# Kernel tuning notes

Hardware: AMD Instinct MI355X
Metric: run time of the kernel (lower is better)

## Reference

```python
import jax, jax.numpy as jnp
import numpy as np

N_NODES = 50000
N_EDGES = 800000
IN_DIM = 128
OUT_DIM = 128
NEG_INIT = -1e9  # matches torch fill_(-1e9) init for scatter amax
LEAKY_SLOPE = 0.01  # nn.LeakyReLU default


def setup_inputs() -> dict:
    key = jax.random.key(0)
    ks = jax.random.split(key, 8)
    x = jax.random.normal(ks[0], (N_NODES, IN_DIM), dtype=jnp.float32)
    edge_index = jax.random.randint(ks[1], (2, N_EDGES), 0, N_NODES, dtype=jnp.int64)
    edge_weight = jax.random.uniform(ks[2], (N_EDGES,), dtype=jnp.float32)
    # MLP params (nn.Linear default init: U(-1/sqrt(fan_in), 1/sqrt(fan_in)))
    s1 = 1.0 / np.sqrt(IN_DIM)
    s2 = 1.0 / np.sqrt(OUT_DIM)
    w1 = jax.random.uniform(ks[3], (OUT_DIM, IN_DIM), minval=-s1, maxval=s1, dtype=jnp.float32)
    b1 = jax.random.uniform(ks[4], (OUT_DIM,), minval=-s1, maxval=s1, dtype=jnp.float32)
    w2 = jax.random.uniform(ks[5], (OUT_DIM, OUT_DIM), minval=-s2, maxval=s2, dtype=jnp.float32)
    b2 = jax.random.uniform(ks[6], (OUT_DIM,), minval=-s2, maxval=s2, dtype=jnp.float32)
    eps = jnp.zeros((1,), dtype=jnp.float32)
    return {"x": x, "edge_index": edge_index, "edge_weight": edge_weight,
            "w1": w1, "b1": b1, "w2": w2, "b2": b2, "eps": eps}


def reference(x, edge_index, edge_weight, w1, b1, w2, b2, eps):
    src = edge_index[0]
    dst = edge_index[1]
    # gather + optional edge-weight scale: [E, D]
    messages = x[src] * edge_weight[:, None]
    # scatter-max to dst; init at -1e9 so include_self=False semantics hold
    agg = jnp.full(x.shape, NEG_INIT, dtype=x.dtype).at[dst].max(messages)
    agg = jnp.where(agg == NEG_INIT, jnp.zeros_like(agg), agg)  # isolated nodes -> 0
    h = (1.0 + eps) * x + agg  # eps broadcasts ([1])
    h = h @ w1.T + b1
    h = jnp.where(h >= 0, h, LEAKY_SLOPE * h)  # LeakyReLU
    out = h @ w2.T + b2
    return out
```

## Files before the change

kernel.cpp:

```cpp
#include <hip/hip_runtime.h>
#include <stdint.h>

#define NN 50000
#define NE 800000
#define D  128
#define NEG_INIT -1e9f
#define CAP 64
#define OVF_CAP 131072

#define CNT_OFF     64
#define OVF_CNT_OFF 50064
#define OVF_OFF     50068
#define BKT_OFF     312320
#define XBF_OFF     3512320
#define WBF_OFF     6712320

#define NBLK 196
#define HSTRIDE 136

typedef __attribute__((ext_vector_type(8))) short short8;
typedef __attribute__((ext_vector_type(4))) float float4v;

__device__ __forceinline__ float b2f(uint16_t u) {
    union { uint32_t u; float f; } v; v.u = ((uint32_t)u) << 16; return v.f;
}
__device__ __forceinline__ uint16_t f2b(float f) {
    union { float f; uint32_t u; } v; v.f = f;
    uint32_t r = v.u + 0x7fffu + ((v.u >> 16) & 1u);
    return (uint16_t)(r >> 16);
}

__device__ __forceinline__ void block_probe(const uint16_t* __restrict__ xraw,
                                            const int* __restrict__ eraw,
                                            int* sflags) {
    int t = threadIdx.x;
    if (t < 64) {
        float v0 = b2f(xraw[2 * t]);
        float v1 = b2f(xraw[2 * t + 1]);
        int bad = (!(v0 > -1e4f && v0 < 1e4f)) || (!(v1 > -1e4f && v1 < 1e4f));
        unsigned long long bm = __ballot(bad);
        int nz = (t < 32) ? (eraw[2 * t + 1] != 0) : 0;
        unsigned long long im = __ballot(nz);
        if (t == 0) { sflags[0] = bm ? 1 : 0; sflags[1] = im ? 0 : 1; }
    }
    __syncthreads();
}

__global__ __launch_bounds__(256) void prep_kernel(
    const uint16_t* __restrict__ xraw,
    const int*      __restrict__ eraw,
    const uint16_t* __restrict__ w1raw,
    const uint16_t* __restrict__ w2raw,
    int* __restrict__ ws)
{
    __shared__ int sflags[2];
    block_probe(xraw, eraw, sflags);
    const int f32 = sflags[0];

    int bid = blockIdx.x;
    if (bid < 6250) {
        int i4 = (bid * 256 + threadIdx.x) * 4;
        ushort* dst = (ushort*)(ws + XBF_OFF);
        if (f32) {
            float4 v = *(const float4*)((const float*)xraw + i4);
            ushort4 o; o.x = f2b(v.x); o.y = f2b(v.y); o.z = f2b(v.z); o.w = f2b(v.w);
            *(ushort4*)(dst + i4) = o;
        } else {
            *(ushort4*)(dst + i4) = *(const ushort4*)(xraw + i4);
        }
    } else if (bid < 6282) {
        int i4 = ((bid - 6250) * 256 + threadIdx.x) * 4;
        const uint16_t* src = (i4 < 16384) ? w1raw : w2raw;
        int off = i4 & 16383;
        ushort* dst = (ushort*)(ws + WBF_OFF);
        if (f32) {
            float4 v = *(const float4*)((const float*)src + off);
            ushort4 o; o.x = f2b(v.x); o.y = f2b(v.y); o.z = f2b(v.z); o.w = f2b(v.w);
            *(ushort4*)(dst + i4) = o;
        } else {
            *(ushort4*)(dst + i4) = *(const ushort4*)(src + off);
        }
    } else {
        int i = (bid - 6282) * 256 + threadIdx.x;
        if (i < NN) ws[CNT_OFF + i] = 0;
        if (i == 0)  ws[OVF_CNT_OFF] = 0;
    }
}

__global__ __launch_bounds__(256) void fill_kernel(
    const uint16_t* __restrict__ xraw,
    const int*      __restrict__ eraw,
    const uint16_t* __restrict__ ewraw,
    int* __restrict__ ws)
{
    __shared__ int sflags[2];
    block_probe(xraw, eraw, sflags);
    const int f32 = sflags[0], i64 = sflags[1];

    int e = blockIdx.x * 256 + threadIdx.x;
    int src, dst;
    if (i64) {
        const long long* e64 = (const long long*)eraw;
        src = (int)e64[e];
        dst = (int)e64[NE + e];
    } else {
        src = eraw[e];
        dst = eraw[NE + e];
    }
    if ((unsigned)src >= NN || (unsigned)dst >= NN) return;
    uint w = f32 ? (uint)f2b(((const float*)ewraw)[e]) : (uint)ewraw[e];
    uint entry = (w << 16) | (uint)src;
    int slot = atomicAdd(ws + CNT_OFF + dst, 1);
    if (slot < CAP) {
        ((uint*)(ws + BKT_OFF))[(size_t)dst * CAP + slot] = entry;
    } else {
        int o = atomicAdd(ws + OVF_CNT_OFF, 1);
        if (o < OVF_CAP) {
            ws[OVF_OFF + 2 * o]     = dst;
            ws[OVF_OFF + 2 * o + 1] = (int)entry;
        }
    }
}

__global__ __launch_bounds__(256) void gmlp_kernel(
    const uint16_t* __restrict__ xraw,
    const int*      __restrict__ eraw,
    const uint16_t* __restrict__ b1raw,
    const uint16_t* __restrict__ b2raw,
    const uint16_t* __restrict__ epsraw,
    const int* __restrict__ ws,
    uint16_t* __restrict__ outraw)
{
    __shared__ int    sflags[2];
    __shared__ uint   tl[16 * (HSTRIDE / 2)];
    __shared__ ushort hl[16 * HSTRIDE];

    block_probe(xraw, eraw, sflags);
    const int f32 = sflags[0];

    const int tid  = threadIdx.x;
    const int wave = tid >> 6;
    const int lane = tid & 63;
    const int m    = lane & 15;
    const int quad = lane >> 4;
    const int node0 = blockIdx.x * 16;

    const ushort* w1b = (const ushort*)(ws + WBF_OFF);
    const ushort* w2b = w1b + 16384;
    const uint*   xbf = (const uint*)(ws + XBF_OFF);
    const uint*   bkt = (const uint*)(ws + BKT_OFF);

    const float eps1 = 1.0f + (f32 ? ((const float*)epsraw)[0] : b2f(epsraw[0]));

    for (int j = 0; j < 4; ++j) {
        int nl = wave * 4 + j;
        int n  = node0 + nl;
        int cnt_raw = ws[CNT_OFF + n];
        int cnt = (cnt_raw < CAP) ? cnt_raw : CAP;

        float m0[16], m1[16];
        #pragma unroll
        for (int u = 0; u < 16; ++u) { m0[u] = NEG_INIT; m1[u] = NEG_INIT; }

        const uint* brow = bkt + (size_t)n * CAP;
        for (int i = 0; i < cnt; i += 16) {
            uint4 q[4];
            #pragma unroll
            for (int qq = 0; qq < 4; ++qq) q[qq] = *(const uint4*)(brow + i + qq * 4);
            #pragma unroll
            for (int u = 0; u < 16; ++u) {
                uint e0 = ((const uint*)q)[u];
                bool ok = (i + u) < cnt;
                uint idx = ok ? (e0 & 0xffffu) : 0u;
                uint v = xbf[idx * 64 + lane];
                float w  = b2f((uint16_t)(e0 >> 16));
                float p0 = b2f((uint16_t)v) * w;
                float p1 = b2f((uint16_t)(v >> 16)) * w;
                m0[u] = fmaxf(m0[u], ok ? p0 : NEG_INIT);
                m1[u] = fmaxf(m1[u], ok ? p1 : NEG_INIT);
            }
        }
        if (cnt_raw > CAP) {
            int novf = ws[OVF_CNT_OFF];
            if (novf > OVF_CAP) novf = OVF_CAP;
            for (int o = 0; o < novf; ++o) {
                if (ws[OVF_OFF + 2 * o] == n) {
                    uint e0 = (uint)ws[OVF_OFF + 2 * o + 1];
                    uint v  = xbf[(e0 & 0xffff) * 64 + lane];
                    float w = b2f((uint16_t)(e0 >> 16));
                    m0[0] = fmaxf(m0[0], b2f((uint16_t)v) * w);
                    m1[0] = fmaxf(m1[0], b2f((uint16_t)(v >> 16)) * w);
                }
            }
        }
        #pragma unroll
        for (int u = 8; u > 0; u >>= 1)
            #pragma unroll
            for (int v2 = 0; v2 < u; ++v2) {
                m0[v2] = fmaxf(m0[v2], m0[v2 + u]);
                m1[v2] = fmaxf(m1[v2], m1[v2 + u]);
            }
        float mx = m0[0], my = m1[0];
        if (cnt_raw == 0) { mx = 0.f; my = 0.f; }

        uint xv = xbf[(size_t)n * 64 + lane];
        float t0 = eps1 * b2f((uint16_t)xv) + mx;
        float t1 = eps1 * b2f((uint16_t)(xv >> 16)) + my;
        tl[nl * (HSTRIDE / 2) + lane] = (uint)f2b(t0) | ((uint)f2b(t1) << 16);
    }
    __syncthreads();

    short8 a[4];
    {
        const ushort* arow = (const ushort*)tl + m * HSTRIDE + quad * 8;
        #pragma unroll
        for (int kb = 0; kb < 4; ++kb) a[kb] = *(const short8*)(arow + kb * 32);
    }

    #pragma unroll
    for (int t = 0; t < 2; ++t) {
        int ct = wave * 2 + t;
        float4v c = {0.f, 0.f, 0.f, 0.f};
        const ushort* brow = w1b + (size_t)(ct * 16 + m) * 128 + quad * 8;
        #pragma unroll
        for (int kb = 0; kb < 4; ++kb)
            c = __builtin_amdgcn_mfma_f32_16x16x32_bf16(a[kb], *(const short8*)(brow + kb * 32), c, 0, 0, 0);
        float bias = f32 ? ((const float*)b1raw)[ct * 16 + m] : b2f(b1raw[ct * 16 + m]);
        #pragma unroll
        for (int r = 0; r < 4; ++r) {
            float v = c[r] + bias;
            v = (v >= 0.f) ? v : 0.01f * v;
            hl[(quad * 4 + r) * HSTRIDE + ct * 16 + m] = f2b(v);
        }
    }
    __syncthreads();

    short8 ah[4];
    {
        const ushort* hrow = hl + m * HSTRIDE + quad * 8;
        #pragma unroll
        for (int kb = 0; kb < 4; ++kb) ah[kb] = *(const short8*)(hrow + kb * 32);
    }

    #pragma unroll
    for (int t = 0; t < 2; ++t) {
        int ct = wave * 2 + t;
        float4v c = {0.f, 0.f, 0.f, 0.f};
        const ushort* brow = w2b + (size_t)(ct * 16 + m) * 128 + quad * 8;
        #pragma unroll
        for (int kb = 0; kb < 4; ++kb)
            c = __builtin_amdgcn_mfma_f32_16x16x32_bf16(ah[kb], *(const short8*)(brow + kb * 32), c, 0, 0, 0);
        float bias = f32 ? ((const float*)b2raw)[ct * 16 + m] : b2f(b2raw[ct * 16 + m]);
        #pragma unroll
        for (int r = 0; r < 4; ++r) {
            float v = c[r] + bias;
            size_t o = (size_t)(node0 + quad * 4 + r) * 128 + ct * 16 + m;
            if (f32) ((float*)outraw)[o] = v;
            else     outraw[o] = f2b(v);
        }
    }
}

extern "C" void kernel_launch(void* const* d_in, const int* in_sizes, int n_in,
                              void* d_out, int out_size, void* d_ws, size_t ws_size,
                              hipStream_t stream) {
    const uint16_t* x    = (const uint16_t*)d_in[0];
    const int*      eidx = (const int*)     d_in[1];
    const uint16_t* ew   = (const uint16_t*)d_in[2];
    const uint16_t* w1   = (const uint16_t*)d_in[3];
    const uint16_t* b1   = (const uint16_t*)d_in[4];
    const uint16_t* w2   = (const uint16_t*)d_in[5];
    const uint16_t* b2   = (const uint16_t*)d_in[6];
    const uint16_t* eps  = (const uint16_t*)d_in[7];
    uint16_t*       out  = (uint16_t*)d_out;
    int* ws = (int*)d_ws;

    prep_kernel<<<6250 + 32 + NBLK, 256, 0, stream>>>(x, eidx, w1, w2, ws);
    fill_kernel<<<NE / 256, 256, 0, stream>>>(x, eidx, ew, ws);
    gmlp_kernel<<<NN / 16, 256, 0, stream>>>(x, eidx, b1, b2, eps, ws, out);
}
```

Measured before the change: 209.8 us.

## Bucket edges by source slice so gathers sweep x in cache-friendly phases

The per-destination buckets are split into four cells, one per quarter of the source-node range, and the gather kernel walks the slices in lockstep with a block barrier after each. Blocks running together then read source rows from the same quarter of x, which is meant to keep the gather working set in L2/MALL. The inner loop is also reshaped into a 4-wide overlapping window instead of a 16-wide masked unroll. In exchange it adds four times the counters and bucket cells, more atomic contention spread, extra barriers, and a higher overflow risk, since each cell holds only 20 entries.

```diff
diff --git a/kernel.cpp b/kernel.cpp
--- a/kernel.cpp
+++ b/kernel.cpp
@@ -5,17 +5,19 @@
 #define NE 800000
 #define D  128
 #define NEG_INIT -1e9f
-#define CAP 64
+#define NS 4
+#define SLICE 12500
+#define CAPS 20
 #define OVF_CAP 131072
 
 #define CNT_OFF     64
-#define OVF_CNT_OFF 50064
-#define OVF_OFF     50068
-#define BKT_OFF     312320
-#define XBF_OFF     3512320
-#define WBF_OFF     6712320
-
-#define NBLK 196
+#define OVF_CNT_OFF 200064
+#define OVF_OFF     200068
+#define BKT_OFF     462336
+#define XBF_OFF     4462336
+#define WBF_OFF     7662336
+
+#define NBLKC 782
 #define HSTRIDE 136
 
 typedef __attribute__((ext_vector_type(8))) short short8;
@@ -82,8 +84,8 @@
         }
     } else {
         int i = (bid - 6282) * 256 + threadIdx.x;
-        if (i < NN) ws[CNT_OFF + i] = 0;
-        if (i == 0)  ws[OVF_CNT_OFF] = 0;
+        if (i < NN * NS) ws[CNT_OFF + i] = 0;
+        if (i == NN * NS) ws[OVF_CNT_OFF] = 0;
     }
 }
 
@@ -110,9 +112,11 @@
     if ((unsigned)src >= NN || (unsigned)dst >= NN) return;
     uint w = f32 ? (uint)f2b(((const float*)ewraw)[e]) : (uint)ewraw[e];
     uint entry = (w << 16) | (uint)src;
-    int slot = atomicAdd(ws + CNT_OFF + dst, 1);
-    if (slot < CAP) {
-        ((uint*)(ws + BKT_OFF))[(size_t)dst * CAP + slot] = entry;
+    int s = src / SLICE;
+    int cell = dst * NS + s;
+    int slot = atomicAdd(ws + CNT_OFF + cell, 1);
+    if (slot < CAPS) {
+        ((uint*)(ws + BKT_OFF))[(size_t)cell * CAPS + slot] = entry;
     } else {
         int o = atomicAdd(ws + OVF_CNT_OFF, 1);
         if (o < OVF_CAP) {
@@ -152,57 +156,86 @@
 
     const float eps1 = 1.0f + (f32 ? ((const float*)epsraw)[0] : b2f(epsraw[0]));
 
+    float acc0[4], acc1[4];
+    int   tot[4];
+    int   ovf_any = 0;
+    #pragma unroll
+    for (int j = 0; j < 4; ++j) { acc0[j] = NEG_INIT; acc1[j] = NEG_INIT; tot[j] = 0; }
+
+    for (int s = 0; s < NS; ++s) {
+        #pragma unroll
+        for (int j = 0; j < 4; ++j) {
+            int n = node0 + wave * 4 + j;
+            int cell = n * NS + s;
+            int cr = ws[CNT_OFF + cell];
+            tot[j] += cr;
+            if (cr > CAPS) ovf_any = 1;
+            int cc = (cr < CAPS) ? cr : CAPS;
+            const uint* brow = bkt + (size_t)cell * CAPS;
+
+            if (cc >= 4) {
+                int i = 0;
+                while (true) {
+                    uint e0 = brow[i], e1 = brow[i + 1], e2 = brow[i + 2], e3 = brow[i + 3];
+                    uint v0 = xbf[(e0 & 0xffffu) * 64 + lane];
+                    uint v1 = xbf[(e1 & 0xffffu) * 64 + lane];
+                    uint v2 = xbf[(e2 & 0xffffu) * 64 + lane];
+                    uint v3 = xbf[(e3 & 0xffffu) * 64 + lane];
+                    float w0 = b2f((uint16_t)(e0 >> 16)), w1v = b2f((uint16_t)(e1 >> 16));
+                    float w2v = b2f((uint16_t)(e2 >> 16)), w3 = b2f((uint16_t)(e3 >> 16));
+                    float q0 = fmaxf(b2f((uint16_t)v0) * w0, b2f((uint16_t)v1) * w1v);
+                    float q1 = fmaxf(b2f((uint16_t)v2) * w2v, b2f((uint16_t)v3) * w3);
+                    acc0[j] = fmaxf(acc0[j], fmaxf(q0, q1));
+                    float r0 = fmaxf(b2f((uint16_t)(v0 >> 16)) * w0, b2f((uint16_t)(v1 >> 16)) * w1v);
+                    float r1 = fmaxf(b2f((uint16_t)(v2 >> 16)) * w2v, b2f((uint16_t)(v3 >> 16)) * w3);
+                    acc1[j] = fmaxf(acc1[j], fmaxf(r0, r1));
+                    i += 4;
+                    if (i >= cc) break;
+                    if (i + 4 > cc) i = cc - 4;
+                }
+            } else if (cc > 0) {
+                uint e0 = brow[0], e1 = brow[1], e2 = brow[2], e3 = brow[3];
+                uint ee[4] = {e0, e1, e2, e3};
+                #pragma unroll
+                for (int u = 0; u < 4; ++u) {
+                    uint v = xbf[(ee[u] & 0xffffu) * 64 + lane];
+                    float w  = b2f((uint16_t)(ee[u] >> 16));
+                    bool ok = u < cc;
+                    float p0 = b2f((uint16_t)v) * w;
+                    float p1 = b2f((uint16_t)(v >> 16)) * w;
+                    acc0[j] = fmaxf(acc0[j], ok ? p0 : NEG_INIT);
+                    acc1[j] = fmaxf(acc1[j], ok ? p1 : NEG_INIT);
+                }
+            }
+        }
+        __syncthreads();
+    }
+
+    if (ovf_any) {
+        int novf = ws[OVF_CNT_OFF];
+        if (novf > OVF_CAP) novf = OVF_CAP;
+        for (int o = 0; o < novf; ++o) {
+            int dsto = ws[OVF_OFF + 2 * o];
+            #pragma unroll
+            for (int j = 0; j < 4; ++j) {
+                int n = node0 + wave * 4 + j;
+                if (dsto == n) {
+                    uint e0 = (uint)ws[OVF_OFF + 2 * o + 1];
+                    uint v  = xbf[(e0 & 0xffff) * 64 + lane];
+                    float w = b2f((uint16_t)(e0 >> 16));
+                    acc0[j] = fmaxf(acc0[j], b2f((uint16_t)v) * w);
+                    acc1[j] = fmaxf(acc1[j], b2f((uint16_t)(v >> 16)) * w);
+                }
+            }
+        }
+    }
+
+    #pragma unroll
     for (int j = 0; j < 4; ++j) {
         int nl = wave * 4 + j;
         int n  = node0 + nl;
-        int cnt_raw = ws[CNT_OFF + n];
-        int cnt = (cnt_raw < CAP) ? cnt_raw : CAP;
-
-        float m0[16], m1[16];
-        #pragma unroll
-        for (int u = 0; u < 16; ++u) { m0[u] = NEG_INIT; m1[u] = NEG_INIT; }
-
-        const uint* brow = bkt + (size_t)n * CAP;
-        for (int i = 0; i < cnt; i += 16) {
-            uint4 q[4];
-            #pragma unroll
-            for (int qq = 0; qq < 4; ++qq) q[qq] = *(const uint4*)(brow + i + qq * 4);
-            #pragma unroll
-            for (int u = 0; u < 16; ++u) {
-                uint e0 = ((const uint*)q)[u];
-                bool ok = (i + u) < cnt;
-                uint idx = ok ? (e0 & 0xffffu) : 0u;
-                uint v = xbf[idx * 64 + lane];
-                float w  = b2f((uint16_t)(e0 >> 16));
-                float p0 = b2f((uint16_t)v) * w;
-                float p1 = b2f((uint16_t)(v >> 16)) * w;
-                m0[u] = fmaxf(m0[u], ok ? p0 : NEG_INIT);
-                m1[u] = fmaxf(m1[u], ok ? p1 : NEG_INIT);
-            }
-        }
-        if (cnt_raw > CAP) {
-            int novf = ws[OVF_CNT_OFF];
-            if (novf > OVF_CAP) novf = OVF_CAP;
-            for (int o = 0; o < novf; ++o) {
-                if (ws[OVF_OFF + 2 * o] == n) {
-                    uint e0 = (uint)ws[OVF_OFF + 2 * o + 1];
-                    uint v  = xbf[(e0 & 0xffff) * 64 + lane];
-                    float w = b2f((uint16_t)(e0 >> 16));
-                    m0[0] = fmaxf(m0[0], b2f((uint16_t)v) * w);
-                    m1[0] = fmaxf(m1[0], b2f((uint16_t)(v >> 16)) * w);
-                }
-            }
-        }
-        #pragma unroll
-        for (int u = 8; u > 0; u >>= 1)
-            #pragma unroll
-            for (int v2 = 0; v2 < u; ++v2) {
-                m0[v2] = fmaxf(m0[v2], m0[v2 + u]);
-                m1[v2] = fmaxf(m1[v2], m1[v2 + u]);
-            }
-        float mx = m0[0], my = m1[0];
-        if (cnt_raw == 0) { mx = 0.f; my = 0.f; }
-
+        float mx = acc0[j], my = acc1[j];
+        if (tot[j] == 0) { mx = 0.f; my = 0.f; }
         uint xv = xbf[(size_t)n * 64 + lane];
         float t0 = eps1 * b2f((uint16_t)xv) + mx;
         float t1 = eps1 * b2f((uint16_t)(xv >> 16)) + my;
@@ -275,7 +308,7 @@
     uint16_t*       out  = (uint16_t*)d_out;
     int* ws = (int*)d_ws;
 
-    prep_kernel<<<6250 + 32 + NBLK, 256, 0, stream>>>(x, eidx, w1, w2, ws);
+    prep_kernel<<<6250 + 32 + NBLKC, 256, 0, stream>>>(x, eidx, w1, w2, ws);
     fill_kernel<<<NE / 256, 256, 0, stream>>>(x, eidx, ew, ws);
     gmlp_kernel<<<NN / 16, 256, 0, stream>>>(x, eidx, b1, b2, eps, ws, out);
 }
```

Result: slower. 215.6 us (+2.8%).
